# Kernel tuning notes

Measured on AMD Instinct MI355X. Metric: run time of the kernel, lower is better.

Reference implementation:

```python
import jax, jax.numpy as jnp
import numpy as np

N_SAMPLES = 32768


def fft_shift(a, shift):
    n = a.shape[-1]
    shift_samples = shift * (n / 3.0)  # trailing dim of shift is 1 -> broadcasts over coeffs
    pad = [(0, 0)] * (a.ndim - 1) + [(0, 2 * n)]
    spec = jnp.fft.rfft(jnp.pad(a, pad), axis=-1, norm='ortho')
    n_coeffs = spec.shape[-1]
    phase = jnp.arange(n_coeffs) * (2j * jnp.pi / n_coeffs)
    spec = spec * jnp.exp(-phase * shift_samples)
    out = jnp.fft.irfft(spec, n=3 * n, axis=-1, norm='ortho')
    return out[..., :n]


def interp_linear(x, out_size):
    # matches torch F.interpolate(mode='linear', align_corners=False)
    in_size = x.shape[-1]
    scale = in_size / out_size
    coords = (jnp.arange(out_size, dtype=x.dtype) + 0.5) * scale - 0.5
    coords = jnp.clip(coords, 0.0, in_size - 1)
    i0 = jnp.floor(coords).astype(jnp.int32)
    i1 = jnp.minimum(i0 + 1, in_size - 1)
    w = coords - i0.astype(x.dtype)
    return x[..., i0] * (1.0 - w) + x[..., i1] * w


def instrument(t, shift, energy, properties):
    batch, n_events, time_len = t.shape
    t = fft_shift(t, shift)  # (b,e,T)
    _, _, cp, n_frames = energy.shape
    frame_shifts = jnp.linspace(0.0, 1.0, n_frames)
    # (b,e,1,T) shifted per-frame -> (b,e,F,T)
    exp_t = fft_shift(t[:, :, None, :], frame_shifts[None, None, :, None])
    exp_t = exp_t[:, :, None, :, :]  # (b,e,1,F,T)
    # triu mask with offset 2: mask[i,j]=1 iff j >= i+2
    mask = (jnp.arange(time_len)[None, :] >= (jnp.arange(n_frames)[:, None] + 2)).astype(t.dtype)
    mask = fft_shift(mask[None, None], shift[:, :, None, :])  # (b,e,F,T)
    mass = properties[..., :1, None]      # (b,e,cp,1,1)
    friction = properties[..., 1:, None]  # (b,e,cp,1,1)
    x = energy[..., None] * jnp.exp(-friction / (2.0 * mass) * exp_t)  # (b,e,cp,F,T)
    x = x * mask[:, :, None, :, :]
    return jnp.sum(x, axis=-2)  # (b,e,cp,T)


def reference(time, shifts, energy, shape, properties, w_pos, b_pos, w_layers, b_layers):
    batch, n_events, cp, n_frames = energy.shape
    channels, enc = w_pos.shape
    # positional filterbank -> embed -> (1,1,channels,N)
    freqs = jnp.linspace(1e-05, 0.5, enc)
    tt = jnp.linspace(0.0, float(N_SAMPLES), N_SAMPLES)
    p = jnp.sin(tt[:, None] * freqs[None, :] * jnp.pi)  # (N, enc)
    pos = (p @ w_pos.T + b_pos).T[None, None]  # (1,1,channels,N)
    # envelopes
    env = instrument(time, shifts, energy, properties)  # (b,e,cp,T)
    env = jax.nn.relu(interp_linear(env, N_SAMPLES))    # (b,e,cp,N)
    # shape network (residual layers use only l2: x + l2(relu(x)))
    s = jnp.swapaxes(shape, -1, -2)  # (b,e,F,channels)
    for i in range(w_layers.shape[0]):
        s = s + jax.nn.relu(s) @ w_layers[i].T + b_layers[i]
    s = jax.nn.relu(s)
    s = jnp.swapaxes(s, -1, -2)           # (b,e,channels,F)
    s = interp_linear(s, N_SAMPLES)       # (b,e,channels,N)
    x = pos * s * env                      # cp == channels
    return jnp.sum(x, axis=2)              # (b,e,N)


def setup_inputs():
    key = jax.random.key(0)
    ks = jax.random.split(key, 9)
    B, E, CP, F_, T, CH, ENC, L = 2, 8, 32, 64, 2048, 32, 256, 4
    return {
        'time': jax.random.uniform(ks[0], (B, E, T), dtype=jnp.float32),
        'shifts': jax.random.uniform(ks[1], (B, E, 1), dtype=jnp.float32),
        'energy': jax.random.uniform(ks[2], (B, E, CP, F_), dtype=jnp.float32),
        'shape': jax.random.normal(ks[3], (B, E, CH, F_), dtype=jnp.float32),
        'properties': jax.random.uniform(ks[4], (B, E, CP, 2), dtype=jnp.float32) + 0.5,
        'w_pos': jax.random.normal(ks[5], (CH, ENC), dtype=jnp.float32) * 0.06,
        'b_pos': jax.random.normal(ks[6], (CH,), dtype=jnp.float32) * 0.02,
        'w_layers': jax.random.normal(ks[7], (L, CH, CH), dtype=jnp.float32) * 0.15,
        'b_layers': jax.random.normal(ks[8], (L, CH), dtype=jnp.float32) * 0.02,
    }
```

## Files before the change

kernel.cpp:

```cpp
#include <hip/hip_runtime.h>
#include <math.h>

#define TL 2048
#define PI_D 3.14159265358979323846

typedef __attribute__((ext_vector_type(8))) short short8v;
typedef __attribute__((ext_vector_type(4))) float float4v;

#define REPB 784
#define OFF_B 8192

__device__ __forceinline__ unsigned short bf16_rne(float f) {
  unsigned u = __float_as_uint(f);
  return (unsigned short)((u + 0x7FFFu + ((u >> 16) & 1u)) >> 16);
}

__device__ __forceinline__ float tap_val(int idx, double beta, double wv) {
  int d = idx - 2047;
  double x = PI_D * (double)d / 6144.0 - beta;
  if (fabs(x) < 1e-9) return 1.0f;
  double c = wv * (cos(x) / sin(x));
  if (d & 1) c = -c;
  return (float)c;
}

__global__ __launch_bounds__(256) void build_shift_k(const float* __restrict__ shifts,
                                                     const float* __restrict__ time_in,
                                                     const float* __restrict__ w_pos,
                                                     float* __restrict__ kerC,
                                                     unsigned short* __restrict__ BFrep,
                                                     unsigned short* __restrict__ tsh_b,
                                                     unsigned short* __restrict__ Whl) {
  __shared__ __align__(16) unsigned char sm1[17408];
  __shared__ float wsum[4];
  int b = blockIdx.x;
  int tid = threadIdx.x;
  if (b < 80) {
    float* kf = (float*)sm1;
    double s;
    if (b < 64) s = (double)b * (1.0 / 63.0) * (2048.0 / 3.0);
    else        s = (double)shifts[b - 64] * (2048.0 / 3.0);
    double beta = PI_D * s / 3073.0;
    double y = 3072.0 * s / 3073.0;
    double r = y - rint(y);
    double wv = -sin(2.0 * PI_D * r) / 6144.0;
    for (int idx = tid; idx < 4104; idx += 256)
      kf[idx] = (idx < 4095) ? tap_val(idx, beta, wv) : 0.0f;
    __syncthreads();
    if (b < 64) {
      for (int c = tid; c < 4096; c += 256) {
        int sr = c >> 9;
        int m = c & 511;
        int A = 4095 - 8 * m + sr;
        unsigned short out[8];
#pragma unroll
        for (int rr = 0; rr < 8; ++rr) out[rr] = bf16_rne(kf[A - rr]);
        *(short8v*)(BFrep + ((size_t)(b * 8 + sr)) * 4104 + 8 * m) = *(short8v*)out;
      }
    } else {
      float s0 = 0.f;
      int base = tid * 16;
#pragma unroll
      for (int i = 0; i < 16; ++i) s0 += kf[base + i];
      int lane = tid & 63;
      float v = s0;
#pragma unroll
      for (int d = 1; d < 64; d <<= 1) {
        float o = __shfl_up(v, (unsigned)d, 64);
        if (lane >= d) v += o;
      }
      if (lane == 63) wsum[tid >> 6] = v;
      __syncthreads();
      float woff = 0.f;
      for (int k = 0; k < (tid >> 6); ++k) woff += wsum[k];
      float run = v + woff - s0;
      float* crow = kerC + (b - 64) * 4096;
#pragma unroll
      for (int i = 0; i < 16; ++i) {
        crow[base + i] = run;
        run += kf[base + i];
      }
    }
  } else if (b < 336) {
    int idx = b - 80;
    int p = idx >> 4, tile = idx & 15;
    int t0 = tile * 128;
    float* a = (float*)sm1;
    float* kw = (float*)(sm1 + 8192);
    float* partial = (float*)(sm1 + 16896);
    double s = (double)shifts[p] * (2048.0 / 3.0);
    double beta = PI_D * s / 3073.0;
    double y = 3072.0 * s / 3073.0;
    double r = y - rint(y);
    double wv = -sin(2.0 * PI_D * r) / 6144.0;
    for (int i = tid; i < 2048; i += 256) a[i] = time_in[p * 2048 + i];
    for (int i = tid; i < 2175; i += 256) kw[i] = tap_val(t0 + i, beta, wv);
    __syncthreads();
    int tl = tid & 127, uh = tid >> 7;
    int base = tl + 2047 - (uh << 10);
    int u0 = uh << 10;
    float acc = 0.f;
#pragma unroll 8
    for (int u2 = 0; u2 < 1024; ++u2) acc = fmaf(a[u0 + u2], kw[base - u2], acc);
    __syncthreads();
    if (uh == 1) partial[tl] = acc;
    __syncthreads();
    if (uh == 0) {
      acc += partial[tl];
      tsh_b[p * 2048 + t0 + tl] = bf16_rne(acc);
    }
  } else {
    int c0 = (b - 336) * 1024 + tid * 4;
#pragma unroll
    for (int k2 = 0; k2 < 4; ++k2) {
      int c = c0 + k2;
      int sel = c & 1, g = (c >> 1) & 3, p16v = (c >> 3) & 15;
      int kc = (c >> 7) & 7, ct = c >> 10;
      const float* wrow = w_pos + (ct * 16 + p16v) * 256 + kc * 32 + g * 8;
      short8v ov;
#pragma unroll
      for (int i = 0; i < 8; ++i) {
        float vv = wrow[i];
        unsigned short hb = bf16_rne(vv);
        if (sel == 0) ov[i] = (short)hb;
        else {
          float hf = __uint_as_float(((unsigned)hb) << 16);
          ov[i] = (short)bf16_rne(vv - hf);
        }
      }
      *(short8v*)(Whl + (size_t)c * 8) = ov;
    }
  }
}

__global__ __launch_bounds__(256, 4) void fused_k(const unsigned short* __restrict__ tsh_b,
                                                  const unsigned short* __restrict__ BFrep,
                                                  float* __restrict__ expT,
                                                  const unsigned short* __restrict__ Whl,
                                                  const float* __restrict__ b_pos,
                                                  float* __restrict__ pos,
                                                  const float* __restrict__ shape,
                                                  const float* __restrict__ w_layers,
                                                  const float* __restrict__ b_layers,
                                                  float* __restrict__ s64) {
  __shared__ __align__(16) unsigned char smem[21248];
  int bx = blockIdx.x;
  int tid = threadIdx.x;
  if (bx < 1024) {
    int j = bx & 63;
    int tB = (bx >> 6) << 7;
    int l = tid & 63, w = tid >> 6;
    int p16 = l & 15, g = l >> 4;
    int srep = l & 7, hb = (l >> 3) & 1;
    int h = w >> 1, kp = w & 1;
    int kc0 = kp << 2;

    float4v acc[4];
#pragma unroll
    for (int i = 0; i < 4; ++i) acc[i] = (float4v){0.f, 0.f, 0.f, 0.f};
    int bB2 = OFF_B + srep * REPB + 256 - (hb << 4) + (g << 4) - (h << 7);
    const unsigned short* grow = BFrep + (size_t)j * 8 * 4104;

    for (int ph = 0; ph < 8; ++ph) {
      int ub = ph << 8;
      int Q8 = 1912 - tB + ub;
      __syncthreads();
#pragma unroll
      for (int it = 0; it < 2; ++it) {
        int c = tid + (it << 8);
        int pp = c >> 5, m = c & 31;
        short8v v = *(const short8v*)(tsh_b + pp * 2048 + ub + (m << 3));
        int dst = ((pp << 9) + (m << 4)) ^ ((pp & 7) << 4);
        *(short8v*)(smem + dst) = v;
      }
      for (int c = tid; c < 384; c += 256) {
        int sr = c / 48;
        int m = c - sr * 48;
        short8v v = *(const short8v*)(grow + sr * 4104 + 8 + Q8 + (m << 3));
        *(short8v*)(smem + OFF_B + sr * REPB + (m << 4)) = v;
      }
      __syncthreads();
      int fb = bB2 + (kc0 << 6);
      short8v W0 = *(const short8v*)(smem + fb);
      short8v W1 = *(const short8v*)(smem + fb - 32);
      short8v W2 = *(const short8v*)(smem + fb - 64);
      short8v W3 = *(const short8v*)(smem + fb - 96);
#pragma unroll
      for (int qq = 0; qq < 4; ++qq) {
        int kc = kc0 + qq;
        if (qq > 0) {
          short8v t2 = W0, t3 = W1;
          W0 = *(const short8v*)(smem + fb + (qq << 6));
          W1 = *(const short8v*)(smem + fb + (qq << 6) - 32);
          W2 = t2;
          W3 = t3;
        }
        int ao = ((p16 << 9) + (kc << 6) + (g << 4)) ^ ((p16 & 7) << 4);
        short8v a = *(const short8v*)(smem + ao);
        acc[0] = __builtin_amdgcn_mfma_f32_16x16x32_bf16(a, W0, acc[0], 0, 0, 0);
        acc[1] = __builtin_amdgcn_mfma_f32_16x16x32_bf16(a, W1, acc[1], 0, 0, 0);
        acc[2] = __builtin_amdgcn_mfma_f32_16x16x32_bf16(a, W2, acc[2], 0, 0, 0);
        acc[3] = __builtin_amdgcn_mfma_f32_16x16x32_bf16(a, W3, acc[3], 0, 0, 0);
      }
    }
    __syncthreads();
    if (kp == 1) {
#pragma unroll
      for (int ct = 0; ct < 4; ++ct)
        *(float4v*)(smem + ((((h << 2) + ct) << 6) + l) * 16) = acc[ct];
    }
    __syncthreads();
    if (kp == 0) {
#pragma unroll
      for (int ct = 0; ct < 4; ++ct) {
        float4v o = *(const float4v*)(smem + ((((h << 2) + ct) << 6) + l) * 16);
#pragma unroll
        for (int rr = 0; rr < 4; ++rr) acc[ct][rr] += o[rr];
      }
      int tbase = tB + (h << 6) + p16;
#pragma unroll
      for (int ct = 0; ct < 4; ++ct) {
#pragma unroll
        for (int rr = 0; rr < 4; ++rr) {
          int prow = (g << 2) + rr;
          expT[(size_t)(prow * 64 + j) * TL + tbase + (ct << 4)] = acc[ct][rr];
        }
      }
    }
  } else if (bx < 1040) {
    float(*sA)[33] = (float(*)[33])(smem);
    float(*sB)[33] = (float(*)[33])(smem + 8448);
    float(*W)[33] = (float(*)[33])(smem + 16896);
    float* bb = (float*)(smem + 21120);
    int p = bx - 1024;
    for (int idx = tid; idx < 2048; idx += 256) {
      int c = idx >> 6, f = idx & 63;
      sA[f][c] = shape[p * 2048 + idx];
    }
    int c = tid & 31, fg = tid >> 5;
    for (int ll = 0; ll < 4; ++ll) {
      for (int idx = tid; idx < 1024; idx += 256) W[idx >> 5][idx & 31] = w_layers[ll * 1024 + idx];
      if (tid < 32) bb[tid] = b_layers[ll * 32 + tid];
      __syncthreads();
      float(*cur)[33] = (ll & 1) ? sB : sA;
      float(*nxt)[33] = (ll & 1) ? sA : sB;
#pragma unroll
      for (int i = 0; i < 8; ++i) {
        int f = fg * 8 + i;
        float acc = cur[f][c] + bb[c];
#pragma unroll
        for (int k = 0; k < 32; ++k) acc = fmaf(fmaxf(cur[f][k], 0.f), W[c][k], acc);
        nxt[f][c] = acc;
      }
      __syncthreads();
    }
    for (int idx = tid; idx < 2048; idx += 256) {
      int cc = idx >> 6, f = idx & 63;
      s64[p * 2048 + idx] = fmaxf(sA[f][cc], 0.f);
    }
  } else {
    int l = tid & 63, w = tid >> 6;
    int p16 = l & 15, g = l >> 4;
    int T0 = (bx - 1040) * 64 + w * 16;

    float ttv = (float)(T0 + p16) * (32768.0f / 32767.0f);
    float4v acc0 = {0.f, 0.f, 0.f, 0.f};
    float4v acc1 = {0.f, 0.f, 0.f, 0.f};
    const short8v* Wt = (const short8v*)Whl;
    int fbase = (p16 << 3) + (g << 1);
#pragma unroll
    for (int kc = 0; kc < 8; ++kc) {
      short8v bh0 = Wt[(kc << 7) + fbase];
      short8v bl0 = Wt[(kc << 7) + fbase + 1];
      short8v bh1 = Wt[1024 + (kc << 7) + fbase];
      short8v bl1 = Wt[1024 + (kc << 7) + fbase + 1];
      short8v ahi, alo;
#pragma unroll
      for (int i = 0; i < 8; ++i) {
        int f = kc * 32 + g * 8 + i;
        float fr = 1e-5f + (float)f * ((0.5f - 1e-5f) / 255.0f);
        float rev = ttv * (0.5f * fr);
        float sv = __builtin_amdgcn_sinf(__builtin_amdgcn_fractf(rev));
        unsigned short hbit = bf16_rne(sv);
        float hf = __uint_as_float(((unsigned)hbit) << 16);
        ahi[i] = (short)hbit;
        alo[i] = (short)bf16_rne(sv - hf);
      }
      acc0 = __builtin_amdgcn_mfma_f32_16x16x32_bf16(ahi, bh0, acc0, 0, 0, 0);
      acc1 = __builtin_amdgcn_mfma_f32_16x16x32_bf16(ahi, bh1, acc1, 0, 0, 0);
      acc0 = __builtin_amdgcn_mfma_f32_16x16x32_bf16(ahi, bl0, acc0, 0, 0, 0);
      acc1 = __builtin_amdgcn_mfma_f32_16x16x32_bf16(ahi, bl1, acc1, 0, 0, 0);
      acc0 = __builtin_amdgcn_mfma_f32_16x16x32_bf16(alo, bh0, acc0, 0, 0, 0);
      acc1 = __builtin_amdgcn_mfma_f32_16x16x32_bf16(alo, bh1, acc1, 0, 0, 0);
    }
    float bp0 = b_pos[p16], bp1 = b_pos[16 + p16];
    float4v o0, o1;
#pragma unroll
    for (int rr = 0; rr < 4; ++rr) {
      o0[rr] = acc0[rr] + bp0;
      o1[rr] = acc1[rr] + bp1;
    }
    int Tr = T0 + g * 4;
    *(float4v*)(pos + (size_t)p16 * 32768 + Tr) = o0;
    *(float4v*)(pos + (size_t)(16 + p16) * 32768 + Tr) = o1;
  }
}

__global__ __launch_bounds__(256) void env2_k(const float* __restrict__ energy,
                                              const float* __restrict__ props,
                                              const float* __restrict__ expT,
                                              const float* __restrict__ kerC,
                                              float* __restrict__ env) {
  int p = blockIdx.x >> 5, tile = blockIdx.x & 31;
  int tl = threadIdx.x & 63;
  int cg = threadIdx.x >> 6;
  int tC = tile * 64;
  int t = tC + tl;
  __shared__ float Et[64][36];
  __shared__ float K[32];
  __shared__ float kcl[2112];
  for (int i = threadIdx.x; i < 2048; i += 256) Et[i & 63][i >> 6] = energy[p * 2048 + i];
  const float* crow = kerC + p * 4096;
  for (int i = threadIdx.x; i < 2110; i += 256) kcl[i] = crow[tC + i];
  if (threadIdx.x < 32) {
    float mass = props[(p * 32 + threadIdx.x) * 2];
    float fric = props[(p * 32 + threadIdx.x) * 2 + 1];
    K[threadIdx.x] = fric / (2.0f * mass);
  }
  __syncthreads();
  float acc[8];
  float kk[8];
#pragma unroll
  for (int i = 0; i < 8; ++i) acc[i] = 0.f;
#pragma unroll
  for (int i = 0; i < 8; ++i) kk[i] = K[cg * 8 + i];
  float Ct = kcl[tl];
  const float* xrow = expT + (size_t)p * 64 * TL + t;
  for (int jj = 0; jj < 64; ++jj) {
    float x = xrow[jj * TL];
    float mv = kcl[tl + 2046 - jj] - Ct;
    float4v e0 = *(const float4v*)(&Et[jj][cg * 8]);
    float4v e1 = *(const float4v*)(&Et[jj][cg * 8 + 4]);
#pragma unroll
    for (int cc = 0; cc < 4; ++cc)
      acc[cc] = fmaf(e0[cc] * mv, __expf(-kk[cc] * x), acc[cc]);
#pragma unroll
    for (int cc = 0; cc < 4; ++cc)
      acc[4 + cc] = fmaf(e1[cc] * mv, __expf(-kk[4 + cc] * x), acc[4 + cc]);
  }
#pragma unroll
  for (int cc = 0; cc < 8; ++cc)
    env[(size_t)(p * 32 + cg * 8 + cc) * TL + t] = acc[cc];
}

__global__ __launch_bounds__(256) void final_k(const float* __restrict__ pos,
                                               const float* __restrict__ s64,
                                               const float* __restrict__ env,
                                               float* __restrict__ out) {
  int gid = blockIdx.x * 256 + threadIdx.x;
  int p = gid >> 15, T = gid & 32767;
  float ft = (float)T + 0.5f;
  float ce = fminf(fmaxf(ft * 0.0625f - 0.5f, 0.f), 2047.f);
  int ie = (int)ce;
  int ie1 = min(ie + 1, 2047);
  float we = ce - (float)ie;
  float cs = fminf(fmaxf(ft * (1.0f / 512.0f) - 0.5f, 0.f), 63.f);
  int is0 = (int)cs;
  int is1 = min(is0 + 1, 63);
  float ws = cs - (float)is0;
  const float* erow = env + (size_t)p * 32 * TL;
  const float* srow = s64 + p * 32 * 64;
  float acc = 0.f;
  for (int c = 0; c < 32; ++c) {
    float pv = pos[(size_t)c * 32768 + T];
    float ev = fmaxf(erow[c * TL + ie] * (1.f - we) + erow[c * TL + ie1] * we, 0.f);
    float sv = srow[c * 64 + is0] * (1.f - ws) + srow[c * 64 + is1] * ws;
    acc += pv * sv * ev;
  }
  out[gid] = acc;
}

extern "C" void kernel_launch(void* const* d_in, const int* in_sizes, int n_in,
                              void* d_out, int out_size, void* d_ws, size_t ws_size,
                              hipStream_t stream) {
  const float* time_in  = (const float*)d_in[0];
  const float* shifts   = (const float*)d_in[1];
  const float* energy   = (const float*)d_in[2];
  const float* shape    = (const float*)d_in[3];
  const float* props    = (const float*)d_in[4];
  const float* w_pos    = (const float*)d_in[5];
  const float* b_pos    = (const float*)d_in[6];
  const float* w_layers = (const float*)d_in[7];
  const float* b_layers = (const float*)d_in[8];

  float* ws = (float*)d_ws;
  float* kerC = ws;
  unsigned short* BFrep = (unsigned short*)(ws + 65536);
  unsigned short* tsh_b = (unsigned short*)(ws + 1116160);
  float* expT = ws + 1132544;
  float* pos  = ws + 3229696;
  float* s64  = ws + 4278272;
  unsigned short* Whl = (unsigned short*)(ws + 4311040);
  float* env  = ws + 4327424;
  float* out  = (float*)d_out;

  hipLaunchKernelGGL(build_shift_k, dim3(340), dim3(256), 0, stream,
                     shifts, time_in, w_pos, kerC, BFrep, tsh_b, Whl);
  hipLaunchKernelGGL(fused_k, dim3(1552), dim3(256), 0, stream, tsh_b, BFrep, expT,
                     Whl, b_pos, pos, shape, w_layers, b_layers, s64);
  hipLaunchKernelGGL(env2_k, dim3(512), dim3(256), 0, stream, energy, props, expT, kerC, env);
  hipLaunchKernelGGL(final_k, dim3(2048), dim3(256), 0, stream, pos, s64, env, out);
}
```

Measured before the change: 94.30 us.

## Restructure Toeplitz MFMA kernel into split-K blocks with single-shot LDS staging

The shift-convolution MFMA kernel now uses 512-thread blocks. Each block covers a 512-wide time tile and one half of the K range. It stages its whole A slice and the Toeplitz band into LDS once, instead of in eight synchronized phases. The two K halves write separate partial expT buffers, which env2_k sums on load. This removes the intra-block reduction and the repeated barriers. In exchange it doubles expT writes and reads, uses more LDS per block, and reorders the side workloads in the grid.

```diff
diff --git a/kernel.cpp b/kernel.cpp
--- a/kernel.cpp
+++ b/kernel.cpp
@@ -7,8 +7,9 @@
 typedef __attribute__((ext_vector_type(8))) short short8v;
 typedef __attribute__((ext_vector_type(4))) float float4v;
 
-#define REPB 784
-#define OFF_B 8192
+#define BROW 4144
+#define BSTRIDE 3168
+#define A_BYTES 32768
 
 __device__ __forceinline__ unsigned short bf16_rne(float f) {
   unsigned u = __float_as_uint(f);
@@ -48,14 +49,19 @@
       kf[idx] = (idx < 4095) ? tap_val(idx, beta, wv) : 0.0f;
     __syncthreads();
     if (b < 64) {
-      for (int c = tid; c < 4096; c += 256) {
-        int sr = c >> 9;
-        int m = c & 511;
-        int A = 4095 - 8 * m + sr;
-        unsigned short out[8];
-#pragma unroll
-        for (int rr = 0; rr < 8; ++rr) out[rr] = bf16_rne(kf[A - rr]);
-        *(short8v*)(BFrep + ((size_t)(b * 8 + sr)) * 4104 + 8 * m) = *(short8v*)out;
+      int sr = tid >> 5, lane5 = tid & 31;
+#pragma unroll
+      for (int it = 0; it < 17; ++it) {
+        int m = lane5 + (it << 5);
+        if (m < 518) {
+          unsigned short out[8];
+#pragma unroll
+          for (int i = 0; i < 8; ++i) {
+            int arg = 4095 - (8 * m + i) + sr;
+            out[i] = (arg >= 0) ? bf16_rne(kf[arg]) : (unsigned short)0;
+          }
+          *(short8v*)(BFrep + ((size_t)(b * 8 + sr)) * BROW + 8 * m) = *(short8v*)out;
+        }
       }
     } else {
       float s0 = 0.f;
@@ -133,135 +139,86 @@
   }
 }
 
-__global__ __launch_bounds__(256, 4) void fused_k(const unsigned short* __restrict__ tsh_b,
-                                                  const unsigned short* __restrict__ BFrep,
-                                                  float* __restrict__ expT,
-                                                  const unsigned short* __restrict__ Whl,
-                                                  const float* __restrict__ b_pos,
-                                                  float* __restrict__ pos,
-                                                  const float* __restrict__ shape,
-                                                  const float* __restrict__ w_layers,
-                                                  const float* __restrict__ b_layers,
-                                                  float* __restrict__ s64) {
-  __shared__ __align__(16) unsigned char smem[21248];
+__global__ __launch_bounds__(512, 4) void fused3_k(const unsigned short* __restrict__ tsh_b,
+                                                   const unsigned short* __restrict__ BFrep,
+                                                   float* __restrict__ expTh,
+                                                   const unsigned short* __restrict__ Whl,
+                                                   const float* __restrict__ b_pos,
+                                                   float* __restrict__ pos,
+                                                   const float* __restrict__ shape,
+                                                   const float* __restrict__ w_layers,
+                                                   const float* __restrict__ b_layers,
+                                                   float* __restrict__ s64) {
+  __shared__ __align__(16) unsigned char smem[A_BYTES + 8 * BSTRIDE];
   int bx = blockIdx.x;
   int tid = threadIdx.x;
-  if (bx < 1024) {
+  if (bx < 512) {
     int j = bx & 63;
-    int tB = (bx >> 6) << 7;
+    int kh = (bx >> 6) & 1;
+    int tQ = bx >> 7;
     int l = tid & 63, w = tid >> 6;
     int p16 = l & 15, g = l >> 4;
-    int srep = l & 7, hb = (l >> 3) & 1;
-    int h = w >> 1, kp = w & 1;
-    int kc0 = kp << 2;
+    int srep = p16 & 7, hb = p16 >> 3;
+    const unsigned short* grow = BFrep + (size_t)j * 8 * BROW;
+    int z_lo = 1536 - 512 * tQ + 1024 * kh;
+
+#pragma unroll
+    for (int it = 0; it < 4; ++it) {
+      int c = tid + (it << 9);
+      int pp = c >> 7, m = c & 127;
+      short8v v = *(const short8v*)(tsh_b + pp * 2048 + kh * 1024 + (m << 3));
+      int dst = ((pp << 11) + (m << 4)) ^ ((pp & 7) << 4);
+      *(short8v*)(smem + dst) = v;
+    }
+    {
+      int sr = tid >> 6, lane6 = tid & 63;
+      const unsigned short* srcrow = grow + sr * BROW + z_lo;
+      unsigned char* dstrow = smem + A_BYTES + sr * BSTRIDE;
+#pragma unroll
+      for (int it = 0; it < 4; ++it) {
+        int m = lane6 + (it << 6);
+        if (m < 197) {
+          short8v v = *(const short8v*)(srcrow + (m << 3));
+          *(short8v*)(dstrow + (m << 4)) = v;
+        }
+      }
+    }
+    __syncthreads();
 
     float4v acc[4];
 #pragma unroll
     for (int i = 0; i < 4; ++i) acc[i] = (float4v){0.f, 0.f, 0.f, 0.f};
-    int bB2 = OFF_B + srep * REPB + 256 - (hb << 4) + (g << 4) - (h << 7);
-    const unsigned short* grow = BFrep + (size_t)j * 8 * 4104;
-
-    for (int ph = 0; ph < 8; ++ph) {
-      int ub = ph << 8;
-      int Q8 = 1912 - tB + ub;
-      __syncthreads();
-#pragma unroll
-      for (int it = 0; it < 2; ++it) {
-        int c = tid + (it << 8);
-        int pp = c >> 5, m = c & 31;
-        short8v v = *(const short8v*)(tsh_b + pp * 2048 + ub + (m << 3));
-        int dst = ((pp << 9) + (m << 4)) ^ ((pp & 7) << 4);
-        *(short8v*)(smem + dst) = v;
-      }
-      for (int c = tid; c < 384; c += 256) {
-        int sr = c / 48;
-        int m = c - sr * 48;
-        short8v v = *(const short8v*)(grow + sr * 4104 + 8 + Q8 + (m << 3));
-        *(short8v*)(smem + OFF_B + sr * REPB + (m << 4)) = v;
-      }
-      __syncthreads();
-      int fb = bB2 + (kc0 << 6);
+    int bBbase = A_BYTES + srep * BSTRIDE + 1024 - (w << 7) - (hb << 4) + (g << 4);
+    short8v W2 = *(const short8v*)(smem + bBbase - 64);
+    short8v W3 = *(const short8v*)(smem + bBbase - 96);
+#pragma unroll 4
+    for (int kc = 0; kc < 32; ++kc) {
+      int ao = ((p16 << 11) + (kc << 6) + (g << 4)) ^ ((p16 & 7) << 4);
+      short8v a = *(const short8v*)(smem + ao);
+      int fb = bBbase + (kc << 6);
       short8v W0 = *(const short8v*)(smem + fb);
       short8v W1 = *(const short8v*)(smem + fb - 32);
-      short8v W2 = *(const short8v*)(smem + fb - 64);
-      short8v W3 = *(const short8v*)(smem + fb - 96);
-#pragma unroll
-      for (int qq = 0; qq < 4; ++qq) {
-        int kc = kc0 + qq;
-        if (qq > 0) {
-          short8v t2 = W0, t3 = W1;
-          W0 = *(const short8v*)(smem + fb + (qq << 6));
-          W1 = *(const short8v*)(smem + fb + (qq << 6) - 32);
-          W2 = t2;
-          W3 = t3;
-        }
-        int ao = ((p16 << 9) + (kc << 6) + (g << 4)) ^ ((p16 & 7) << 4);
-        short8v a = *(const short8v*)(smem + ao);
-        acc[0] = __builtin_amdgcn_mfma_f32_16x16x32_bf16(a, W0, acc[0], 0, 0, 0);
-        acc[1] = __builtin_amdgcn_mfma_f32_16x16x32_bf16(a, W1, acc[1], 0, 0, 0);
-        acc[2] = __builtin_amdgcn_mfma_f32_16x16x32_bf16(a, W2, acc[2], 0, 0, 0);
-        acc[3] = __builtin_amdgcn_mfma_f32_16x16x32_bf16(a, W3, acc[3], 0, 0, 0);
-      }
-    }
-    __syncthreads();
-    if (kp == 1) {
-#pragma unroll
-      for (int ct = 0; ct < 4; ++ct)
-        *(float4v*)(smem + ((((h << 2) + ct) << 6) + l) * 16) = acc[ct];
-    }
-    __syncthreads();
-    if (kp == 0) {
-#pragma unroll
-      for (int ct = 0; ct < 4; ++ct) {
-        float4v o = *(const float4v*)(smem + ((((h << 2) + ct) << 6) + l) * 16);
-#pragma unroll
-        for (int rr = 0; rr < 4; ++rr) acc[ct][rr] += o[rr];
-      }
-      int tbase = tB + (h << 6) + p16;
-#pragma unroll
-      for (int ct = 0; ct < 4; ++ct) {
-#pragma unroll
-        for (int rr = 0; rr < 4; ++rr) {
-          int prow = (g << 2) + rr;
-          expT[(size_t)(prow * 64 + j) * TL + tbase + (ct << 4)] = acc[ct][rr];
-        }
-      }
-    }
-  } else if (bx < 1040) {
-    float(*sA)[33] = (float(*)[33])(smem);
-    float(*sB)[33] = (float(*)[33])(smem + 8448);
-    float(*W)[33] = (float(*)[33])(smem + 16896);
-    float* bb = (float*)(smem + 21120);
-    int p = bx - 1024;
-    for (int idx = tid; idx < 2048; idx += 256) {
-      int c = idx >> 6, f = idx & 63;
-      sA[f][c] = shape[p * 2048 + idx];
-    }
-    int c = tid & 31, fg = tid >> 5;
-    for (int ll = 0; ll < 4; ++ll) {
-      for (int idx = tid; idx < 1024; idx += 256) W[idx >> 5][idx & 31] = w_layers[ll * 1024 + idx];
-      if (tid < 32) bb[tid] = b_layers[ll * 32 + tid];
-      __syncthreads();
-      float(*cur)[33] = (ll & 1) ? sB : sA;
-      float(*nxt)[33] = (ll & 1) ? sA : sB;
-#pragma unroll
-      for (int i = 0; i < 8; ++i) {
-        int f = fg * 8 + i;
-        float acc = cur[f][c] + bb[c];
-#pragma unroll
-        for (int k = 0; k < 32; ++k) acc = fmaf(fmaxf(cur[f][k], 0.f), W[c][k], acc);
-        nxt[f][c] = acc;
-      }
-      __syncthreads();
-    }
-    for (int idx = tid; idx < 2048; idx += 256) {
-      int cc = idx >> 6, f = idx & 63;
-      s64[p * 2048 + idx] = fmaxf(sA[f][cc], 0.f);
-    }
-  } else {
+      acc[0] = __builtin_amdgcn_mfma_f32_16x16x32_bf16(a, W0, acc[0], 0, 0, 0);
+      acc[1] = __builtin_amdgcn_mfma_f32_16x16x32_bf16(a, W1, acc[1], 0, 0, 0);
+      acc[2] = __builtin_amdgcn_mfma_f32_16x16x32_bf16(a, W2, acc[2], 0, 0, 0);
+      acc[3] = __builtin_amdgcn_mfma_f32_16x16x32_bf16(a, W3, acc[3], 0, 0, 0);
+      W2 = W0;
+      W3 = W1;
+    }
+    float* dst = expTh + (size_t)kh * (16 * 64 * 2048);
+    int tcb = 512 * tQ + 64 * w + p16;
+#pragma unroll
+    for (int ct = 0; ct < 4; ++ct) {
+#pragma unroll
+      for (int rr = 0; rr < 4; ++rr) {
+        int prow = (g << 2) + rr;
+        dst[(size_t)(prow * 64 + j) * TL + tcb + (ct << 4)] = acc[ct][rr];
+      }
+    }
+  } else if (bx < 768) {
     int l = tid & 63, w = tid >> 6;
     int p16 = l & 15, g = l >> 4;
-    int T0 = (bx - 1040) * 64 + w * 16;
+    int T0 = (bx - 512) * 128 + w * 16;
 
     float ttv = (float)(T0 + p16) * (32768.0f / 32767.0f);
     float4v acc0 = {0.f, 0.f, 0.f, 0.f};
@@ -303,12 +260,43 @@
     int Tr = T0 + g * 4;
     *(float4v*)(pos + (size_t)p16 * 32768 + Tr) = o0;
     *(float4v*)(pos + (size_t)(16 + p16) * 32768 + Tr) = o1;
+  } else {
+    float(*sA)[33] = (float(*)[33])(smem);
+    float(*sB)[33] = (float(*)[33])(smem + 8448);
+    float(*W)[33] = (float(*)[33])(smem + 16896);
+    float* bb = (float*)(smem + 25344);
+    int p = bx - 768;
+    for (int idx = tid; idx < 2048; idx += 512) {
+      int c = idx >> 6, f = idx & 63;
+      sA[f][c] = shape[p * 2048 + idx];
+    }
+    int c = tid & 31, fg = tid >> 5;
+    for (int ll = 0; ll < 4; ++ll) {
+      for (int idx = tid; idx < 1024; idx += 512) W[idx >> 5][idx & 31] = w_layers[ll * 1024 + idx];
+      if (tid < 32) bb[tid] = b_layers[ll * 32 + tid];
+      __syncthreads();
+      float(*cur)[33] = (ll & 1) ? sB : sA;
+      float(*nxt)[33] = (ll & 1) ? sA : sB;
+#pragma unroll
+      for (int i = 0; i < 4; ++i) {
+        int f = fg * 4 + i;
+        float acc = cur[f][c] + bb[c];
+#pragma unroll
+        for (int k = 0; k < 32; ++k) acc = fmaf(fmaxf(cur[f][k], 0.f), W[c][k], acc);
+        nxt[f][c] = acc;
+      }
+      __syncthreads();
+    }
+    for (int idx = tid; idx < 2048; idx += 512) {
+      int cc = idx >> 6, f = idx & 63;
+      s64[p * 2048 + idx] = fmaxf(sA[f][cc], 0.f);
+    }
   }
 }
 
 __global__ __launch_bounds__(256) void env2_k(const float* __restrict__ energy,
                                               const float* __restrict__ props,
-                                              const float* __restrict__ expT,
+                                              const float* __restrict__ expTh,
                                               const float* __restrict__ kerC,
                                               float* __restrict__ env) {
   int p = blockIdx.x >> 5, tile = blockIdx.x & 31;
@@ -335,9 +323,10 @@
 #pragma unroll
   for (int i = 0; i < 8; ++i) kk[i] = K[cg * 8 + i];
   float Ct = kcl[tl];
-  const float* xrow = expT + (size_t)p * 64 * TL + t;
+  const float* xrow0 = expTh + (size_t)p * 64 * TL + t;
+  const float* xrow1 = xrow0 + (size_t)16 * 64 * TL;
   for (int jj = 0; jj < 64; ++jj) {
-    float x = xrow[jj * TL];
+    float x = xrow0[jj * TL] + xrow1[jj * TL];
     float mv = kcl[tl + 2046 - jj] - Ct;
     float4v e0 = *(const float4v*)(&Et[jj][cg * 8]);
     float4v e1 = *(const float4v*)(&Et[jj][cg * 8 + 4]);
@@ -396,18 +385,18 @@
   float* ws = (float*)d_ws;
   float* kerC = ws;
   unsigned short* BFrep = (unsigned short*)(ws + 65536);
-  unsigned short* tsh_b = (unsigned short*)(ws + 1116160);
-  float* expT = ws + 1132544;
-  float* pos  = ws + 3229696;
-  float* s64  = ws + 4278272;
-  unsigned short* Whl = (unsigned short*)(ws + 4311040);
-  float* env  = ws + 4327424;
+  unsigned short* tsh_b = (unsigned short*)(ws + 1126400);
+  float* expTh = ws + 1142784;
+  float* pos  = ws + 5337088;
+  float* s64  = ws + 6385664;
+  unsigned short* Whl = (unsigned short*)(ws + 6418432);
+  float* env  = ws + 6434816;
   float* out  = (float*)d_out;
 
   hipLaunchKernelGGL(build_shift_k, dim3(340), dim3(256), 0, stream,
                      shifts, time_in, w_pos, kerC, BFrep, tsh_b, Whl);
-  hipLaunchKernelGGL(fused_k, dim3(1552), dim3(256), 0, stream, tsh_b, BFrep, expT,
+  hipLaunchKernelGGL(fused3_k, dim3(784), dim3(512), 0, stream, tsh_b, BFrep, expTh,
                      Whl, b_pos, pos, shape, w_layers, b_layers, s64);
-  hipLaunchKernelGGL(env2_k, dim3(512), dim3(256), 0, stream, energy, props, expT, kerC, env);
+  hipLaunchKernelGGL(env2_k, dim3(512), dim3(256), 0, stream, energy, props, expTh, kerC, env);
   hipLaunchKernelGGL(final_k, dim3(2048), dim3(256), 0, stream, pos, s64, env, out);
 }
```

Result: faster. 89.22 us (-5.4%).
